# Optimization experiments

Hardware: AMD Instinct MI355X
Metric: run time of the kernel (lower is better)

## Reference

```python
import jax, jax.numpy as jnp
import numpy as np

HIDDEN = 128
VEL_SCALE = 0.5
T_END = 1.0


def conv1x1(x, w, b):
    # x: [B, Cin, N], w: [Cout, Cin], b: [Cout]
    return jnp.einsum('oi,bin->bon', w, x) + b[None, :, None]


def setup_inputs() -> dict:
    key = jax.random.key(0)
    ks = jax.random.split(key, 11)
    B, N = 8, 50000
    def winit(k, shape, fan_in):
        bound = 1.0 / np.sqrt(fan_in)
        return jax.random.uniform(k, shape, jnp.float32, -bound, bound)
    return {
        'x0': jax.random.normal(ks[0], (B, 3, N), jnp.float32),
        'h1_w': winit(ks[1], (HIDDEN, 4), 4), 'h1_b': winit(ks[2], (HIDDEN,), 4),
        'g1_w': winit(ks[3], (HIDDEN, 4), 4), 'g1_b': winit(ks[4], (HIDDEN,), 4),
        'h2_w': winit(ks[5], (HIDDEN, HIDDEN), HIDDEN), 'h2_b': winit(ks[6], (HIDDEN,), HIDDEN),
        'g2_w': winit(ks[7], (HIDDEN, HIDDEN), HIDDEN), 'g2_b': winit(ks[8], (HIDDEN,), HIDDEN),
        'out_w': winit(ks[9], (3, HIDDEN), HIDDEN), 'out_b': winit(ks[10], (3,), HIDDEN),
    }


def field(t, x, h1_w, h1_b, g1_w, g1_b, h2_w, h2_b, g2_w, g2_b, out_w, out_b):
    B, _, N = x.shape
    t_chan = jnp.broadcast_to(jnp.reshape(t, (1, 1, 1)), (B, 1, N))
    z = jnp.concatenate([x, t_chan], axis=1)                 # [B, 4, N]
    z = conv1x1(z, h1_w, h1_b) * jax.nn.sigmoid(conv1x1(z, g1_w, g1_b))
    z = jax.nn.relu(z)
    z = conv1x1(z, h2_w, h2_b) * jax.nn.sigmoid(conv1x1(z, g2_w, g2_b))
    z = jax.nn.relu(z)
    v = conv1x1(z, out_w, out_b)                             # [B, 3, N]
    return jnp.tanh(v) * VEL_SCALE


def reference(x0, h1_w, h1_b, g1_w, g1_b, h2_w, h2_b, g2_w, g2_b, out_w, out_b):
    params = (h1_w, h1_b, g1_w, g1_b, h2_w, h2_b, g2_w, g2_b, out_w, out_b)
    f = lambda t, y: field(jnp.asarray(t, jnp.float32), y, *params)
    # torchdiffeq 'rk4' with t=[0, T] and no step_size: single 3/8-rule RK4 step, h = T
    h = jnp.float32(T_END)
    t0 = jnp.float32(0.0)
    third = jnp.float32(1.0 / 3.0)
    k1 = f(t0, x0)
    k2 = f(t0 + h * third, x0 + h * k1 * third)
    k3 = f(t0 + h * third * 2.0, x0 + h * (k2 - k1 * third))
    k4 = f(t0 + h, x0 + h * (k1 - k2 + k3))
    return x0 + h * (k1 + 3.0 * (k2 + k3) + k4) * jnp.float32(0.125)
```

## Files before the change

### kernel.cpp

```cpp
#include <hip/hip_runtime.h>
#include <math.h>
#include <utility>

typedef __attribute__((ext_vector_type(8))) short    bf16x8;
typedef __attribute__((ext_vector_type(4))) float    f32x4;
typedef __attribute__((ext_vector_type(2))) float    f32x2;
typedef __attribute__((ext_vector_type(2))) unsigned u32x2;
typedef __attribute__((ext_vector_type(4))) unsigned u32x4;

template<int I, int N, class F>
__device__ __forceinline__ void sfor(F&& f) {
    if constexpr (I < N) { f(std::integral_constant<int, I>{}); sfor<I + 1, N>(static_cast<F&&>(f)); }
}

#define NPT    50000
#define NTILES 6250
#define TPB    2
#define Z_S    128
#define LOG2E  1.4426950408889634f

static __device__ __forceinline__ unsigned short bf16r(float f) {
    unsigned u = __builtin_bit_cast(unsigned, f);
    u += 0x7FFFu + ((u >> 16) & 1u);
    return (unsigned short)(u >> 16);
}

#if defined(__has_builtin)
#if __has_builtin(__builtin_amdgcn_cvt_pk_bf16_f32)
#define HAVE_CVT_PK_BF16 1
#endif
#if __has_builtin(__builtin_amdgcn_exp2f) && __has_builtin(__builtin_amdgcn_rcpf)
#define HAVE_RAW_TRANS 1
#endif
#endif

static __device__ __forceinline__ unsigned packbf(float a, float b) {
#ifdef HAVE_CVT_PK_BF16
    return __builtin_bit_cast(unsigned, __builtin_amdgcn_cvt_pk_bf16_f32(a, b));
#else
    return (unsigned)bf16r(a) | ((unsigned)bf16r(b) << 16);
#endif
}

#ifdef HAVE_RAW_TRANS
static __device__ __forceinline__ float fexp2(float x) { return __builtin_amdgcn_exp2f(x); }
static __device__ __forceinline__ float frcp(float x)  { return __builtin_amdgcn_rcpf(x); }
#else
static __device__ __forceinline__ float fexp2(float x) { return __exp2f(x); }
static __device__ __forceinline__ float frcp(float x)  { return __frcp_rn(x); }
#endif

static __device__ __forceinline__ unsigned gate2p(f32x2 h, f32x2 gp) {
    f32x2 e;
    e.x = fexp2(gp.x);
    e.y = fexp2(gp.y);
    f32x2 p = e + 1.f;
    float ip = frcp(p.x * p.y);
    f32x2 ps = __builtin_shufflevector(p, p, 1, 0);
    f32x2 z = (h * ps) * ip;
    z = __builtin_elementwise_max(z, f32x2{0.f, 0.f});
    return packbf(z.x, z.y);
}

static __device__ __forceinline__ bf16x8 pack8s(const float* p, float s) {
    f32x4 lo = *reinterpret_cast<const f32x4*>(p);
    f32x4 hi = *reinterpret_cast<const f32x4*>(p + 4);
    u32x4 u = { packbf(lo[0]*s, lo[1]*s), packbf(lo[2]*s, lo[3]*s),
                packbf(hi[0]*s, hi[1]*s), packbf(hi[2]*s, hi[3]*s) };
    return __builtin_bit_cast(bf16x8, u);
}
static __device__ __forceinline__ f32x4 mfma16(bf16x8 a, bf16x8 b, f32x4 c) {
    return __builtin_amdgcn_mfma_f32_16x16x32_bf16(a, b, c, 0, 0, 0);
}

__global__ __launch_bounds__(512, 4) void node_rk4_mfma(
    const float* __restrict__ x0,
    const float* __restrict__ h1_w, const float* __restrict__ h1_b,
    const float* __restrict__ g1_w, const float* __restrict__ g1_b,
    const float* __restrict__ h2_w, const float* __restrict__ h2_b,
    const float* __restrict__ g2_w, const float* __restrict__ g2_b,
    const float* __restrict__ out_w, const float* __restrict__ out_b,
    float* __restrict__ y)
{
    __shared__ __align__(16) short zin[64 * 8];
    __shared__ __align__(16) short z1s[64 * Z_S];
    __shared__ __align__(16) short z2s[64 * Z_S];
    __shared__ __align__(16) short aow_s[4 * 12 * 8];
    __shared__ __align__(16) float bias_s[4 * 128 + 16];
    __shared__ __align__(8)  unsigned a1_s[2 * 256];

    const int tid  = threadIdx.x;
    const int w    = tid >> 6;
    const int lane = tid & 63;
    const int q    = lane >> 4;
    const int m    = lane & 15;

    const int row = 16 * w + m;
    bf16x8 a2h[4], a2g[4];
    sfor<0, 4>([&](auto KS) {
        constexpr int ks = KS.value;
        a2h[ks] = pack8s(h2_w + row * 128 + ks * 32 + q * 8, 1.0f);
        a2g[ks] = pack8s(g2_w + row * 128 + ks * 32 + q * 8, -LOG2E);
    });
    if (tid < 128) {
        const f32x4 t1 = *reinterpret_cast<const f32x4*>(h1_w + tid * 4);
        const f32x4 t2 = *reinterpret_cast<const f32x4*>(g1_w + tid * 4);
        a1_s[tid * 2]           = packbf(t1[0], t1[1]);
        a1_s[tid * 2 + 1]       = packbf(t1[2], t1[3]);
        a1_s[256 + tid * 2]     = packbf(t2[0] * -LOG2E, t2[1] * -LOG2E);
        a1_s[256 + tid * 2 + 1] = packbf(t2[2] * -LOG2E, t2[3] * -LOG2E);
    }
    if (w == 0 && m < 3) {
        sfor<0, 4>([&](auto KS) {
            constexpr int ks = KS.value;
            bf16x8 t = pack8s(out_w + m * 128 + ks * 32 + q * 8, 2.f * LOG2E);
            *reinterpret_cast<bf16x8*>(&aow_s[((ks * 3 + m) * 4 + q) * 8]) = t;
        });
    }
    if (tid < 128) {
        bias_s[tid]       = h1_b[tid];
        bias_s[128 + tid] = g1_b[tid] * -LOG2E;
        bias_s[256 + tid] = h2_b[tid];
        bias_s[384 + tid] = g2_b[tid] * -LOG2E;
    }
    if (tid < 16) bias_s[512 + tid] = (tid < 3) ? out_b[tid] * (2.f * LOG2E) : 0.f;

    if (tid < 64) *reinterpret_cast<u32x4*>(&zin[tid * 8]) = u32x4{0u, 0u, 0u, 0u};
    __syncthreads();

    const float third = 1.0f / 3.0f;
    const int cb4 = 16 * w + 4 * q;

    const int m7   = m & 7;
    const int qx8  = (q ^ (m & 3)) * 8;
    const int m4_8 = (m & 4) * 8;

    const short* zin_rd = &zin[m * 8];
    short*       zin_wr = &zin[row * 8];
    const short* z1_re  = &z1s[m * Z_S + qx8 + m4_8];
    const short* z1_ro  = &z1s[m * Z_S + qx8 + (m4_8 ^ 32)];
    short*       z1_wr  = &z1s[m * Z_S + (((2 * w + (q >> 1)) ^ m7) * 8) + (q & 1) * 4];
    short*       z2_wr  = &z2s[m * Z_S + (((2 * w + (q >> 1)) ^ m7) * 8) + (q & 1) * 4];
    const short* z2_re  = &z2s[(16 * w + m) * Z_S + qx8 + m4_8];
    const short* z2_ro  = &z2s[(16 * w + m) * Z_S + qx8 + (m4_8 ^ 32)];
    const short* aow_rd = &aow_s[((m < 3 ? m : 2) * 4 + q) * 8];
    const float* bs     = &bias_s[cb4];
    const float* bsov   = &bias_s[512 + 4 * q];

    #pragma unroll 1
    for (int t2 = 0; t2 < TPB; ++t2) {
        const int tile = blockIdx.x * TPB + t2;

        float xc0 = 0.f, xc1 = 0.f, xc2 = 0.f;
        int gbase = 0;
        if (w < 4 && lane < 16) {
            const int pg = tile * 64 + w * 16 + lane;
            const int bb = pg / NPT;
            const int nn = pg - bb * NPT;
            gbase = bb * 3 * NPT + nn;
            xc0 = x0[gbase]; xc1 = x0[gbase + NPT]; xc2 = x0[gbase + 2 * NPT];
        }
        float k1x=0,k1y=0,k1z=0, k2x=0,k2y=0,k2z=0, k3x=0,k3y=0,k3z=0;
        float ax=0, ay=0, az=0;

        #pragma unroll 1
        for (int s = 0; s < 4; ++s) {
            if (w < 4 && lane < 16) {
                float zi0, zi1, zi2, tt;
                if (s == 0)      { zi0 = xc0; zi1 = xc1; zi2 = xc2; tt = 0.f; }
                else if (s == 1) { zi0 = fmaf(k1x, third, xc0);
                                   zi1 = fmaf(k1y, third, xc1);
                                   zi2 = fmaf(k1z, third, xc2); tt = third; }
                else if (s == 2) { zi0 = xc0 + (k2x - k1x * third);
                                   zi1 = xc1 + (k2y - k1y * third);
                                   zi2 = xc2 + (k2z - k1z * third); tt = 2.f * third; }
                else             { zi0 = xc0 + (k1x - k2x + k3x);
                                   zi1 = xc1 + (k1y - k2y + k3y);
                                   zi2 = xc2 + (k1z - k2z + k3z); tt = 1.f; }
                u32x2 pk = { packbf(zi0, zi1), packbf(zi2, tt) };
                *reinterpret_cast<u32x2*>(zin_wr) = pk;
            }
            __syncthreads();

            {
                bf16x8 a1h = {0,0,0,0,0,0,0,0}, a1g = {0,0,0,0,0,0,0,0};
                if (q == 0) {
                    u32x2 th = *reinterpret_cast<const u32x2*>(&a1_s[row * 2]);
                    u32x2 tg = *reinterpret_cast<const u32x2*>(&a1_s[256 + row * 2]);
                    u32x4 uh = { th[0], th[1], 0u, 0u };
                    u32x4 ug = { tg[0], tg[1], 0u, 0u };
                    a1h = __builtin_bit_cast(bf16x8, uh);
                    a1g = __builtin_bit_cast(bf16x8, ug);
                }
                const f32x4 b1h = *reinterpret_cast<const f32x4*>(bs);
                const f32x4 b1g = *reinterpret_cast<const f32x4*>(bs + 128);
                sfor<0, 4>([&](auto NT) {
                    constexpr int nt = NT.value;
                    bf16x8 bf = *reinterpret_cast<const bf16x8*>(zin_rd + nt * 128);
                    f32x4 ch = mfma16(a1h, bf, b1h);
                    f32x4 cg = mfma16(a1g, bf, b1g);
                    u32x2 pk = { gate2p(f32x2{ch[0], ch[1]}, f32x2{cg[0], cg[1]}),
                                 gate2p(f32x2{ch[2], ch[3]}, f32x2{cg[2], cg[3]}) };
                    *reinterpret_cast<u32x2*>(z1_wr + nt * 2048) = pk;
                });
            }
            __syncthreads();

            {
                const f32x4 b2h = *reinterpret_cast<const f32x4*>(bs + 256);
                const f32x4 b2g = *reinterpret_cast<const f32x4*>(bs + 384);
                f32x4 ch[4], cg[4];
                sfor<0, 4>([&](auto NT) {
                    constexpr int nt = NT.value;
                    bf16x8 bf = *reinterpret_cast<const bf16x8*>(z1_re + nt * 2048);
                    ch[nt] = mfma16(a2h[0], bf, b2h);
                    cg[nt] = mfma16(a2g[0], bf, b2g);
                });
                sfor<1, 4>([&](auto KS) {
                    constexpr int ks = KS.value;
                    const short* zb = (ks & 1) ? z1_ro : z1_re;
                    constexpr int koff = (ks & 2) ? 64 : 0;
                    sfor<0, 4>([&](auto NT) {
                        constexpr int nt = NT.value;
                        bf16x8 bf = *reinterpret_cast<const bf16x8*>(zb + nt * 2048 + koff);
                        ch[nt] = mfma16(a2h[ks], bf, ch[nt]);
                        cg[nt] = mfma16(a2g[ks], bf, cg[nt]);
                    });
                });
                sfor<0, 4>([&](auto NT) {
                    constexpr int nt = NT.value;
                    u32x2 pk = { gate2p(f32x2{ch[nt][0], ch[nt][1]}, f32x2{cg[nt][0], cg[nt][1]}),
                                 gate2p(f32x2{ch[nt][2], ch[nt][3]}, f32x2{cg[nt][2], cg[nt][3]}) };
                    *reinterpret_cast<u32x2*>(z2_wr + nt * 2048) = pk;
                });
            }
            __syncthreads();

            if (w < 4) {
                f32x4 vc = *reinterpret_cast<const f32x4*>(bsov);
                sfor<0, 4>([&](auto KS) {
                    constexpr int ks = KS.value;
                    bf16x8 af = *reinterpret_cast<const bf16x8*>(aow_rd + ks * 96);
                    const short* zb = (ks & 1) ? z2_ro : z2_re;
                    constexpr int koff = (ks & 2) ? 64 : 0;
                    bf16x8 bf = *reinterpret_cast<const bf16x8*>(zb + koff);
                    vc = mfma16(af, bf, vc);
                });
                f32x2 e; e.x = fexp2(vc[0]); e.y = fexp2(vc[1]);
                f32x2 p = e + 1.f;
                const float ipxy = frcp(p.x * p.y);
                const float kx = 0.5f - p.y * ipxy;
                const float ky = 0.5f - p.x * ipxy;
                const float kz = 0.5f - frcp(fexp2(vc[2]) + 1.f);

                if (s == 0)      { k1x=kx;k1y=ky;k1z=kz; ax=kx;ay=ky;az=kz; }
                else if (s == 1) { k2x=kx;k2y=ky;k2z=kz;
                                   ax=fmaf(3.f,kx,ax); ay=fmaf(3.f,ky,ay); az=fmaf(3.f,kz,az); }
                else if (s == 2) { k3x=kx;k3y=ky;k3z=kz;
                                   ax=fmaf(3.f,kx,ax); ay=fmaf(3.f,ky,ay); az=fmaf(3.f,kz,az); }
                else             { ax+=kx; ay+=ky; az+=kz; }
            }
        }

        if (w < 4 && lane < 16) {
            y[gbase]           = fmaf(0.125f, ax, xc0);
            y[gbase + NPT]     = fmaf(0.125f, ay, xc1);
            y[gbase + 2 * NPT] = fmaf(0.125f, az, xc2);
        }
        __syncthreads();
    }
}

extern "C" void kernel_launch(void* const* d_in, const int* in_sizes, int n_in,
                              void* d_out, int out_size, void* d_ws, size_t ws_size,
                              hipStream_t stream) {
    (void)in_sizes; (void)n_in; (void)d_ws; (void)ws_size; (void)out_size;
    const float* x0    = (const float*)d_in[0];
    const float* h1_w  = (const float*)d_in[1];
    const float* h1_b  = (const float*)d_in[2];
    const float* g1_w  = (const float*)d_in[3];
    const float* g1_b  = (const float*)d_in[4];
    const float* h2_w  = (const float*)d_in[5];
    const float* h2_b  = (const float*)d_in[6];
    const float* g2_w  = (const float*)d_in[7];
    const float* g2_b  = (const float*)d_in[8];
    const float* out_w = (const float*)d_in[9];
    const float* out_b = (const float*)d_in[10];
    float* y = (float*)d_out;

    node_rk4_mfma<<<NTILES / TPB, 512, 0, stream>>>(
        x0, h1_w, h1_b, g1_w, g1_b, h2_w, h2_b, g2_w, g2_b, out_w, out_b, y);
}
```

Before: 292.9 us.

## Process both point tiles per RK stage together to halve barriers

Instead of looping over two 64-point tiles one after the other, each block now handles all 128 points in one pass through every RK stage. Stage activations for both tiles live side by side in a larger dynamic LDS buffer, and the k1..k3 slopes are kept in LDS rather than in registers. This halves the number of __syncthreads per block and gives more independent MFMAs between barriers (the layer-2 loop is regrouped into pairs of column tiles). In exchange, LDS per block grows to about 77 KB, which may cut the number of resident blocks per CU below the launch-bounds target.

```diff
diff --git a/kernel.cpp b/kernel.cpp
--- a/kernel.cpp
+++ b/kernel.cpp
@@ -14,10 +14,21 @@
 }
 
 #define NPT    50000
-#define NTILES 6250
-#define TPB    2
+#define NBLK   3125
 #define Z_S    128
 #define LOG2E  1.4426950408889634f
+
+#define OFF_Z1   0
+#define OFF_Z2   32768
+#define OFF_ZIN  65536
+#define OFF_KST  67584
+#define OFF_AOW  73728
+#define OFF_BIAS 74496
+#define OFF_A1   76608
+#define LDS_BYTES 78656
+#define TBZ   8192
+#define TBZIN 512
+#define TBK   768
 
 static __device__ __forceinline__ unsigned short bf16r(float f) {
     unsigned u = __builtin_bit_cast(unsigned, f);
@@ -82,12 +93,14 @@
     const float* __restrict__ out_w, const float* __restrict__ out_b,
     float* __restrict__ y)
 {
-    __shared__ __align__(16) short zin[64 * 8];
-    __shared__ __align__(16) short z1s[64 * Z_S];
-    __shared__ __align__(16) short z2s[64 * Z_S];
-    __shared__ __align__(16) short aow_s[4 * 12 * 8];
-    __shared__ __align__(16) float bias_s[4 * 128 + 16];
-    __shared__ __align__(8)  unsigned a1_s[2 * 256];
+    extern __shared__ char lds_raw[];
+    short*    z1s    = reinterpret_cast<short*>(lds_raw + OFF_Z1);
+    short*    z2s    = reinterpret_cast<short*>(lds_raw + OFF_Z2);
+    short*    zin    = reinterpret_cast<short*>(lds_raw + OFF_ZIN);
+    float*    kst    = reinterpret_cast<float*>(lds_raw + OFF_KST);
+    short*    aow_s  = reinterpret_cast<short*>(lds_raw + OFF_AOW);
+    float*    bias_s = reinterpret_cast<float*>(lds_raw + OFF_BIAS);
+    unsigned* a1_s   = reinterpret_cast<unsigned*>(lds_raw + OFF_A1);
 
     const int tid  = threadIdx.x;
     const int w    = tid >> 6;
@@ -125,7 +138,7 @@
     }
     if (tid < 16) bias_s[512 + tid] = (tid < 3) ? out_b[tid] * (2.f * LOG2E) : 0.f;
 
-    if (tid < 64) *reinterpret_cast<u32x4*>(&zin[tid * 8]) = u32x4{0u, 0u, 0u, 0u};
+    if (tid < 128) *reinterpret_cast<u32x4*>(&zin[tid * 8]) = u32x4{0u, 0u, 0u, 0u};
     __syncthreads();
 
     const float third = 1.0f / 3.0f;
@@ -146,104 +159,133 @@
     const short* aow_rd = &aow_s[((m < 3 ? m : 2) * 4 + q) * 8];
     const float* bs     = &bias_s[cb4];
     const float* bsov   = &bias_s[512 + 4 * q];
+    float*       kbase  = &kst[row * 4];
+
+    float xcA0=0.f, xcA1=0.f, xcA2=0.f, xcB0=0.f, xcB1=0.f, xcB2=0.f;
+    int gbA = 0, gbB = 0;
+    if (w < 4 && lane < 16) {
+        const int pgA = blockIdx.x * 128 + row;
+        const int bbA = pgA / NPT;
+        gbA = bbA * 3 * NPT + (pgA - bbA * NPT);
+        xcA0 = x0[gbA]; xcA1 = x0[gbA + NPT]; xcA2 = x0[gbA + 2 * NPT];
+        const int pgB = pgA + 64;
+        const int bbB = pgB / NPT;
+        gbB = bbB * 3 * NPT + (pgB - bbB * NPT);
+        xcB0 = x0[gbB]; xcB1 = x0[gbB + NPT]; xcB2 = x0[gbB + 2 * NPT];
+    }
+    float axA=0.f, ayA=0.f, azA=0.f, axB=0.f, ayB=0.f, azB=0.f;
 
     #pragma unroll 1
-    for (int t2 = 0; t2 < TPB; ++t2) {
-        const int tile = blockIdx.x * TPB + t2;
-
-        float xc0 = 0.f, xc1 = 0.f, xc2 = 0.f;
-        int gbase = 0;
+    for (int s = 0; s < 4; ++s) {
         if (w < 4 && lane < 16) {
-            const int pg = tile * 64 + w * 16 + lane;
-            const int bb = pg / NPT;
-            const int nn = pg - bb * NPT;
-            gbase = bb * 3 * NPT + nn;
-            xc0 = x0[gbase]; xc1 = x0[gbase + NPT]; xc2 = x0[gbase + 2 * NPT];
+            auto STAGET = [&](auto TT, float x0c, float x1c, float x2c) {
+                constexpr int T = TT.value;
+                const float* kb = kbase + T * TBK;
+                float zi0, zi1, zi2, tt;
+                if (s == 0)      { zi0 = x0c; zi1 = x1c; zi2 = x2c; tt = 0.f; }
+                else if (s == 1) {
+                    f32x4 k1 = *reinterpret_cast<const f32x4*>(kb);
+                    zi0 = fmaf(k1[0], third, x0c);
+                    zi1 = fmaf(k1[1], third, x1c);
+                    zi2 = fmaf(k1[2], third, x2c); tt = third;
+                } else if (s == 2) {
+                    f32x4 k1 = *reinterpret_cast<const f32x4*>(kb);
+                    f32x4 k2 = *reinterpret_cast<const f32x4*>(kb + 256);
+                    zi0 = x0c + (k2[0] - k1[0] * third);
+                    zi1 = x1c + (k2[1] - k1[1] * third);
+                    zi2 = x2c + (k2[2] - k1[2] * third); tt = 2.f * third;
+                } else {
+                    f32x4 k1 = *reinterpret_cast<const f32x4*>(kb);
+                    f32x4 k2 = *reinterpret_cast<const f32x4*>(kb + 256);
+                    f32x4 k3 = *reinterpret_cast<const f32x4*>(kb + 512);
+                    zi0 = x0c + (k1[0] - k2[0] + k3[0]);
+                    zi1 = x1c + (k1[1] - k2[1] + k3[1]);
+                    zi2 = x2c + (k1[2] - k2[2] + k3[2]); tt = 1.f;
+                }
+                u32x2 pk = { packbf(zi0, zi1), packbf(zi2, tt) };
+                *reinterpret_cast<u32x2*>(zin_wr + T * TBZIN) = pk;
+            };
+            STAGET(std::integral_constant<int, 0>{}, xcA0, xcA1, xcA2);
+            STAGET(std::integral_constant<int, 1>{}, xcB0, xcB1, xcB2);
         }
-        float k1x=0,k1y=0,k1z=0, k2x=0,k2y=0,k2z=0, k3x=0,k3y=0,k3z=0;
-        float ax=0, ay=0, az=0;
-
-        #pragma unroll 1
-        for (int s = 0; s < 4; ++s) {
-            if (w < 4 && lane < 16) {
-                float zi0, zi1, zi2, tt;
-                if (s == 0)      { zi0 = xc0; zi1 = xc1; zi2 = xc2; tt = 0.f; }
-                else if (s == 1) { zi0 = fmaf(k1x, third, xc0);
-                                   zi1 = fmaf(k1y, third, xc1);
-                                   zi2 = fmaf(k1z, third, xc2); tt = third; }
-                else if (s == 2) { zi0 = xc0 + (k2x - k1x * third);
-                                   zi1 = xc1 + (k2y - k1y * third);
-                                   zi2 = xc2 + (k2z - k1z * third); tt = 2.f * third; }
-                else             { zi0 = xc0 + (k1x - k2x + k3x);
-                                   zi1 = xc1 + (k1y - k2y + k3y);
-                                   zi2 = xc2 + (k1z - k2z + k3z); tt = 1.f; }
-                u32x2 pk = { packbf(zi0, zi1), packbf(zi2, tt) };
-                *reinterpret_cast<u32x2*>(zin_wr) = pk;
+        __syncthreads();
+
+        {
+            bf16x8 a1h = {0,0,0,0,0,0,0,0}, a1g = {0,0,0,0,0,0,0,0};
+            if (q == 0) {
+                u32x2 th = *reinterpret_cast<const u32x2*>(&a1_s[row * 2]);
+                u32x2 tg = *reinterpret_cast<const u32x2*>(&a1_s[256 + row * 2]);
+                u32x4 uh = { th[0], th[1], 0u, 0u };
+                u32x4 ug = { tg[0], tg[1], 0u, 0u };
+                a1h = __builtin_bit_cast(bf16x8, uh);
+                a1g = __builtin_bit_cast(bf16x8, ug);
             }
-            __syncthreads();
-
-            {
-                bf16x8 a1h = {0,0,0,0,0,0,0,0}, a1g = {0,0,0,0,0,0,0,0};
-                if (q == 0) {
-                    u32x2 th = *reinterpret_cast<const u32x2*>(&a1_s[row * 2]);
-                    u32x2 tg = *reinterpret_cast<const u32x2*>(&a1_s[256 + row * 2]);
-                    u32x4 uh = { th[0], th[1], 0u, 0u };
-                    u32x4 ug = { tg[0], tg[1], 0u, 0u };
-                    a1h = __builtin_bit_cast(bf16x8, uh);
-                    a1g = __builtin_bit_cast(bf16x8, ug);
-                }
-                const f32x4 b1h = *reinterpret_cast<const f32x4*>(bs);
-                const f32x4 b1g = *reinterpret_cast<const f32x4*>(bs + 128);
+            const f32x4 b1h = *reinterpret_cast<const f32x4*>(bs);
+            const f32x4 b1g = *reinterpret_cast<const f32x4*>(bs + 128);
+            auto L1T = [&](auto TT) {
+                constexpr int T = TT.value;
                 sfor<0, 4>([&](auto NT) {
                     constexpr int nt = NT.value;
-                    bf16x8 bf = *reinterpret_cast<const bf16x8*>(zin_rd + nt * 128);
+                    bf16x8 bf = *reinterpret_cast<const bf16x8*>(zin_rd + T * TBZIN + nt * 128);
                     f32x4 ch = mfma16(a1h, bf, b1h);
                     f32x4 cg = mfma16(a1g, bf, b1g);
                     u32x2 pk = { gate2p(f32x2{ch[0], ch[1]}, f32x2{cg[0], cg[1]}),
                                  gate2p(f32x2{ch[2], ch[3]}, f32x2{cg[2], cg[3]}) };
-                    *reinterpret_cast<u32x2*>(z1_wr + nt * 2048) = pk;
+                    *reinterpret_cast<u32x2*>(z1_wr + T * TBZ + nt * 2048) = pk;
                 });
-            }
-            __syncthreads();
-
-            {
-                const f32x4 b2h = *reinterpret_cast<const f32x4*>(bs + 256);
-                const f32x4 b2g = *reinterpret_cast<const f32x4*>(bs + 384);
-                f32x4 ch[4], cg[4];
-                sfor<0, 4>([&](auto NT) {
-                    constexpr int nt = NT.value;
-                    bf16x8 bf = *reinterpret_cast<const bf16x8*>(z1_re + nt * 2048);
-                    ch[nt] = mfma16(a2h[0], bf, b2h);
-                    cg[nt] = mfma16(a2g[0], bf, b2g);
+            };
+            L1T(std::integral_constant<int, 0>{});
+            L1T(std::integral_constant<int, 1>{});
+        }
+        __syncthreads();
+
+        {
+            const f32x4 b2h = *reinterpret_cast<const f32x4*>(bs + 256);
+            const f32x4 b2g = *reinterpret_cast<const f32x4*>(bs + 384);
+            auto L2T = [&](auto TT) {
+                constexpr int T = TT.value;
+                sfor<0, 2>([&](auto NTP) {
+                    constexpr int b0 = T * TBZ + (2 * NTP.value) * 2048;
+                    constexpr int b1 = T * TBZ + (2 * NTP.value + 1) * 2048;
+                    f32x4 c0h, c1h, c0g, c1g;
+                    {
+                        bf16x8 f0 = *reinterpret_cast<const bf16x8*>(z1_re + b0);
+                        bf16x8 f1 = *reinterpret_cast<const bf16x8*>(z1_re + b1);
+                        c0h = mfma16(a2h[0], f0, b2h); c1h = mfma16(a2h[0], f1, b2h);
+                        c0g = mfma16(a2g[0], f0, b2g); c1g = mfma16(a2g[0], f1, b2g);
+                    }
+                    sfor<1, 4>([&](auto KS) {
+                        constexpr int ks = KS.value;
+                        const short* zb = (ks & 1) ? z1_ro : z1_re;
+                        constexpr int koff = (ks & 2) ? 64 : 0;
+                        bf16x8 f0 = *reinterpret_cast<const bf16x8*>(zb + b0 + koff);
+                        bf16x8 f1 = *reinterpret_cast<const bf16x8*>(zb + b1 + koff);
+                        c0h = mfma16(a2h[ks], f0, c0h); c1h = mfma16(a2h[ks], f1, c1h);
+                        c0g = mfma16(a2g[ks], f0, c0g); c1g = mfma16(a2g[ks], f1, c1g);
+                    });
+                    u32x2 pk0 = { gate2p(f32x2{c0h[0], c0h[1]}, f32x2{c0g[0], c0g[1]}),
+                                  gate2p(f32x2{c0h[2], c0h[3]}, f32x2{c0g[2], c0g[3]}) };
+                    *reinterpret_cast<u32x2*>(z2_wr + b0) = pk0;
+                    u32x2 pk1 = { gate2p(f32x2{c1h[0], c1h[1]}, f32x2{c1g[0], c1g[1]}),
+                                  gate2p(f32x2{c1h[2], c1h[3]}, f32x2{c1g[2], c1g[3]}) };
+                    *reinterpret_cast<u32x2*>(z2_wr + b1) = pk1;
                 });
-                sfor<1, 4>([&](auto KS) {
-                    constexpr int ks = KS.value;
-                    const short* zb = (ks & 1) ? z1_ro : z1_re;
-                    constexpr int koff = (ks & 2) ? 64 : 0;
-                    sfor<0, 4>([&](auto NT) {
-                        constexpr int nt = NT.value;
-                        bf16x8 bf = *reinterpret_cast<const bf16x8*>(zb + nt * 2048 + koff);
-                        ch[nt] = mfma16(a2h[ks], bf, ch[nt]);
-                        cg[nt] = mfma16(a2g[ks], bf, cg[nt]);
-                    });
-                });
-                sfor<0, 4>([&](auto NT) {
-                    constexpr int nt = NT.value;
-                    u32x2 pk = { gate2p(f32x2{ch[nt][0], ch[nt][1]}, f32x2{cg[nt][0], cg[nt][1]}),
-                                 gate2p(f32x2{ch[nt][2], ch[nt][3]}, f32x2{cg[nt][2], cg[nt][3]}) };
-                    *reinterpret_cast<u32x2*>(z2_wr + nt * 2048) = pk;
-                });
-            }
-            __syncthreads();
-
-            if (w < 4) {
+            };
+            L2T(std::integral_constant<int, 0>{});
+            L2T(std::integral_constant<int, 1>{});
+        }
+        __syncthreads();
+
+        if (w < 4) {
+            auto OUTT = [&](auto TT, float& ax, float& ay, float& az) {
+                constexpr int T = TT.value;
                 f32x4 vc = *reinterpret_cast<const f32x4*>(bsov);
                 sfor<0, 4>([&](auto KS) {
                     constexpr int ks = KS.value;
                     bf16x8 af = *reinterpret_cast<const bf16x8*>(aow_rd + ks * 96);
                     const short* zb = (ks & 1) ? z2_ro : z2_re;
                     constexpr int koff = (ks & 2) ? 64 : 0;
-                    bf16x8 bf = *reinterpret_cast<const bf16x8*>(zb + koff);
+                    bf16x8 bf = *reinterpret_cast<const bf16x8*>(zb + T * TBZ + koff);
                     vc = mfma16(af, bf, vc);
                 });
                 f32x2 e; e.x = fexp2(vc[0]); e.y = fexp2(vc[1]);
@@ -252,22 +294,24 @@
                 const float kx = 0.5f - p.y * ipxy;
                 const float ky = 0.5f - p.x * ipxy;
                 const float kz = 0.5f - frcp(fexp2(vc[2]) + 1.f);
-
-                if (s == 0)      { k1x=kx;k1y=ky;k1z=kz; ax=kx;ay=ky;az=kz; }
-                else if (s == 1) { k2x=kx;k2y=ky;k2z=kz;
-                                   ax=fmaf(3.f,kx,ax); ay=fmaf(3.f,ky,ay); az=fmaf(3.f,kz,az); }
-                else if (s == 2) { k3x=kx;k3y=ky;k3z=kz;
-                                   ax=fmaf(3.f,kx,ax); ay=fmaf(3.f,ky,ay); az=fmaf(3.f,kz,az); }
-                else             { ax+=kx; ay+=ky; az+=kz; }
-            }
+                if (lane < 16 && s < 3)
+                    *reinterpret_cast<f32x4*>(kbase + T * TBK + s * 256) = f32x4{kx, ky, kz, 0.f};
+                if (s == 0)      { ax = kx; ay = ky; az = kz; }
+                else if (s < 3)  { ax = fmaf(3.f, kx, ax); ay = fmaf(3.f, ky, ay); az = fmaf(3.f, kz, az); }
+                else             { ax += kx; ay += ky; az += kz; }
+            };
+            OUTT(std::integral_constant<int, 0>{}, axA, ayA, azA);
+            OUTT(std::integral_constant<int, 1>{}, axB, ayB, azB);
         }
-
-        if (w < 4 && lane < 16) {
-            y[gbase]           = fmaf(0.125f, ax, xc0);
-            y[gbase + NPT]     = fmaf(0.125f, ay, xc1);
-            y[gbase + 2 * NPT] = fmaf(0.125f, az, xc2);
-        }
-        __syncthreads();
+    }
+
+    if (w < 4 && lane < 16) {
+        y[gbA]           = fmaf(0.125f, axA, xcA0);
+        y[gbA + NPT]     = fmaf(0.125f, ayA, xcA1);
+        y[gbA + 2 * NPT] = fmaf(0.125f, azA, xcA2);
+        y[gbB]           = fmaf(0.125f, axB, xcB0);
+        y[gbB + NPT]     = fmaf(0.125f, ayB, xcB1);
+        y[gbB + 2 * NPT] = fmaf(0.125f, azB, xcB2);
     }
 }
 
@@ -288,6 +332,12 @@
     const float* out_b = (const float*)d_in[10];
     float* y = (float*)d_out;
 
-    node_rk4_mfma<<<NTILES / TPB, 512, 0, stream>>>(
+    static bool attr_set = false;
+    if (!attr_set) {
+        (void)hipFuncSetAttribute(reinterpret_cast<const void*>(&node_rk4_mfma),
+                                  hipFuncAttributeMaxDynamicSharedMemorySize, LDS_BYTES);
+        attr_set = true;
+    }
+    node_rk4_mfma<<<NBLK, 512, LDS_BYTES, stream>>>(
         x0, h1_w, h1_b, g1_w, g1_b, h2_w, h2_b, g2_w, g2_b, out_w, out_b, y);
 }
```

Measured after the change: 279.4 us. 1.05x faster.
